# Kernel tuning notes

Hardware: AMD Instinct MI355X
Metric: run time of the kernel (lower is better)

Reference implementation:

```python
import jax, jax.numpy as jnp
import numpy as np

N_NODES = 50000
N_EDGES = 800000
IN_FEATS = 256
HIDDEN = 256
NUM_CLASSES = 64


def setup_inputs() -> dict:
    key = jax.random.key(0)
    k1, k2, k3, k4 = jax.random.split(key, 4)
    features = jax.random.normal(k1, (N_NODES, IN_FEATS), dtype=jnp.float32)
    edge_index = jax.random.randint(k2, (2, N_EDGES), 0, N_NODES, dtype=jnp.int32)
    W1 = jax.random.normal(k3, (IN_FEATS, HIDDEN), dtype=jnp.float32) * (1.0 / np.sqrt(IN_FEATS))
    b1 = jnp.zeros((HIDDEN,), dtype=jnp.float32)
    W2 = jax.random.normal(k4, (HIDDEN, NUM_CLASSES), dtype=jnp.float32) * (1.0 / np.sqrt(HIDDEN))
    b2 = jnp.zeros((NUM_CLASSES,), dtype=jnp.float32)
    return {"features": features, "edge_index": edge_index, "W1": W1, "b1": b1, "W2": W2, "b2": b2}


def reference(features, edge_index, W1, b1, W2, b2):
    # Two-layer GCN: h = A_hat @ relu(A_hat @ X W1 + b1) W2 + b2
    # A_hat uses symmetric degree normalization 1/sqrt(d_src * d_dst)
    N = features.shape[0]
    src, dst = edge_index[0], edge_index[1]
    ones = jnp.ones((src.shape[0],), dtype=features.dtype)
    deg_out = jax.ops.segment_sum(ones, src, num_segments=N)  # out-degree per node
    deg_in = jax.ops.segment_sum(ones, dst, num_segments=N)   # in-degree per node
    inv_sqrt_out = jax.lax.rsqrt(jnp.maximum(deg_out, 1.0))
    inv_sqrt_in = jax.lax.rsqrt(jnp.maximum(deg_in, 1.0))
    edge_norm = (inv_sqrt_out[src] * inv_sqrt_in[dst])[:, None]  # [E,1]

    def gcn_layer(x, W, b):
        h = x @ W                      # transform first (reduces message width)
        msg = h[src] * edge_norm       # [E, out]
        agg = jax.ops.segment_sum(msg, dst, num_segments=N)
        return agg + b

    h = jax.nn.relu(gcn_layer(features, W1, b1))
    return gcn_layer(h, W2, b2)
```

## Files before the change

kernel.cpp:

```cpp
#include <hip/hip_runtime.h>

#define NN 50000
#define MPAD 50048
#define NE 800000
#define SCAN_BLOCKS 49

typedef short short8 __attribute__((ext_vector_type(8)));
typedef float f32x4 __attribute__((ext_vector_type(4)));

__device__ __forceinline__ unsigned short f2bf(float x) {
    unsigned u = __builtin_bit_cast(unsigned, x);
    u += 0x7FFFu + ((u >> 16) & 1u);
    return (unsigned short)(u >> 16);
}
__device__ __forceinline__ float bf2f(unsigned short h) {
    unsigned u = ((unsigned)h) << 16;
    return __builtin_bit_cast(float, u);
}
__device__ __forceinline__ void gld16(const void* g, void* l) {
    __builtin_amdgcn_global_load_lds(
        (const __attribute__((address_space(1))) unsigned int*)g,
        (__attribute__((address_space(3))) unsigned int*)l, 16, 0, 0);
}
__device__ __forceinline__ void nt_store8(void* p, ushort4 v) {
    __builtin_nontemporal_store(__builtin_bit_cast(unsigned long long, v),
                                (unsigned long long*)p);
}


__global__ __launch_bounds__(256) void count_kernel(const int* __restrict__ src,
    const int* __restrict__ dst, int* __restrict__ cnt_out, int* __restrict__ cnt_in, int E)
{
    int e = blockIdx.x * 256 + threadIdx.x;
    if (e < E) {
        atomicAdd(&cnt_out[src[e]], 1);
        atomicAdd(&cnt_in[dst[e]], 1);
    }
}

__global__ __launch_bounds__(256) void scan_kernel(const int* __restrict__ cnt_in,
    const int* __restrict__ cnt_out, int* __restrict__ bsum, int* __restrict__ rs,
    float* __restrict__ inv_out, float* __restrict__ inv_in)
{
    __shared__ int sm[4];
    __shared__ int sprefix;
    const int b = blockIdx.x, tid = threadIdx.x;
    const int lane = tid & 63, wv = tid >> 6;
    int base = b * 1024 + tid * 4;
    int v[4]; int s = 0;
    #pragma unroll
    for (int i = 0; i < 4; ++i) {
        int idx = base + i;
        v[i] = (idx < NN) ? cnt_in[idx] : 0;
        s += v[i];
    }
    int inc = s;
    #pragma unroll
    for (int off = 1; off < 64; off <<= 1) {
        int u = __shfl_up(inc, off, 64);
        if (lane >= off) inc += u;
    }
    if (lane == 63) sm[wv] = inc;
    __syncthreads();
    if (tid == 0) {
        int btot = sm[0] + sm[1] + sm[2] + sm[3];
        atomicExch(&bsum[b], btot + 1);
    }
    if (tid < 64) {
        int pv = 0;
        if (lane < b) {
            int x;
            do { x = atomicAdd(&bsum[lane], 0); } while (x == 0);
            pv = x - 1;
        }
        #pragma unroll
        for (int off = 1; off < 64; off <<= 1) pv += __shfl_xor(pv, off, 64);
        if (lane == 0) sprefix = pv;
    }
    __syncthreads();
    int wo = 0;
    for (int i = 0; i < wv; ++i) wo += sm[i];
    int run = sprefix + wo + (inc - s);
    #pragma unroll
    for (int i = 0; i < 4; ++i) {
        int idx = base + i;
        if (idx < NN) {
            rs[idx] = run; run += v[i];
            inv_in[idx]  = rsqrtf(fmaxf((float)v[i], 1.0f));
            inv_out[idx] = rsqrtf(fmaxf((float)cnt_out[idx], 1.0f));
        }
    }
}

__global__ __launch_bounds__(256) void fill_kernel(const int* __restrict__ src,
    const int* __restrict__ dst, int* __restrict__ rs, int* __restrict__ csr_src, int E)
{
    int e = blockIdx.x * 256 + threadIdx.x;
    if (e < E) {
        int slot = atomicAdd(&rs[dst[e]], 1);
        csr_src[slot] = src[e];
    }
}

__global__ __launch_bounds__(256) void splitW_kernel(const float* __restrict__ W1,
    const float* __restrict__ W2, unsigned short* __restrict__ W1T,
    unsigned short* __restrict__ W2T)
{
    int i = blockIdx.x * 256 + threadIdx.x;
    const float* W; unsigned short* BT; int N; int ii;
    if (i < 256 * 32) { W = W1; BT = W1T; N = 256; ii = i; }
    else if (i < 256 * 32 + 64 * 32) { W = W2; BT = W2T; N = 64; ii = i - 256 * 32; }
    else return;
    int col = ii >> 5, kc = ii & 31;
    short8 hv, lv;
    #pragma unroll
    for (int j = 0; j < 8; ++j) {
        float x = W[(size_t)(kc * 8 + j) * N + col];
        unsigned short h = f2bf(x);
        hv[j] = (short)h;
        lv[j] = (short)f2bf(x - bf2f(h));
    }
    size_t base = (size_t)col * 512;
    size_t o = (kc >> 3) * 64 + (((kc & 7) ^ (col & 7)) * 8);
    *(short8*)&BT[base + o] = hv;
    *(short8*)&BT[base + 256 + o] = lv;
}

__global__ __launch_bounds__(256) void gemm1_fuse_kernel(const float* __restrict__ X,
    const unsigned short* __restrict__ BT, const float* __restrict__ inv_out,
    unsigned short* __restrict__ C, int M)
{
    constexpr int BN = 128, WN = 64, NF = 4;
    __shared__ unsigned short Ash[128 * 64];
    __shared__ unsigned short Asl[128 * 64];
    __shared__ unsigned short Bsh[BN * 64];
    __shared__ unsigned short Bsl[BN * 64];
    const int tid = threadIdx.x;
    const int w = tid >> 6, lane = tid & 63;
    const int wm = w >> 1, wn = w & 1;
    const int r = lane & 15, kg = lane >> 4;
    const int rowbase = blockIdx.x * 128;
    const int colbase = blockIdx.y * BN;

    f32x4 acc[4][NF] = {};

    for (int kb = 0; kb < 4; ++kb) {
        #pragma unroll
        for (int i = 0; i < 4; ++i) {
            int ct = (w * 4 + i) * 64 + lane;
            int row = ct >> 3, c = ct & 7;
            int grow = rowbase + row; if (grow >= NN) grow = NN - 1;
            const float* sp = X + (size_t)grow * 256 + kb * 64 + c * 8;
            float4 x0 = *(const float4*)sp;
            float4 x1 = *(const float4*)(sp + 4);
            float xs[8] = {x0.x, x0.y, x0.z, x0.w, x1.x, x1.y, x1.z, x1.w};
            short8 hv, lv;
            #pragma unroll
            for (int t = 0; t < 8; ++t) {
                unsigned short h = f2bf(xs[t]);
                hv[t] = (short)h;
                lv[t] = (short)f2bf(xs[t] - bf2f(h));
            }
            int dsto = row * 64 + ((c ^ (row & 7)) * 8);
            *(short8*)&Ash[dsto] = hv;
            *(short8*)&Asl[dsto] = lv;
        }
        #pragma unroll
        for (int i = 0; i < 4; ++i) {
            int ct = (w * 4 + i) * 64 + lane;
            int col = ct >> 3, c = ct & 7;
            size_t goff = (size_t)(colbase + col) * 512 + kb * 64 + c * 8;
            gld16(BT + goff, (unsigned short*)Bsh + (size_t)ct * 8);
            gld16(BT + goff + 256, (unsigned short*)Bsl + (size_t)ct * 8);
        }
        __syncthreads();
        #pragma unroll
        for (int ks = 0; ks < 2; ++ks) {
            short8 ahf[4], alf[4];
            #pragma unroll
            for (int mf = 0; mf < 4; ++mf) {
                int row = wm * 64 + mf * 16 + r;
                int lo = row * 64 + (((ks * 4 + kg) ^ (row & 7)) * 8);
                ahf[mf] = *(const short8*)&Ash[lo];
                alf[mf] = *(const short8*)&Asl[lo];
            }
            #pragma unroll
            for (int nf = 0; nf < NF; ++nf) {
                int col = wn * WN + nf * 16 + r;
                int lo = col * 64 + (((ks * 4 + kg) ^ (col & 7)) * 8);
                short8 bh = *(const short8*)&Bsh[lo];
                short8 bl = *(const short8*)&Bsl[lo];
                #pragma unroll
                for (int mf = 0; mf < 4; ++mf) {
                    acc[mf][nf] = __builtin_amdgcn_mfma_f32_16x16x32_bf16(ahf[mf], bh, acc[mf][nf], 0, 0, 0);
                    acc[mf][nf] = __builtin_amdgcn_mfma_f32_16x16x32_bf16(alf[mf], bh, acc[mf][nf], 0, 0, 0);
                    acc[mf][nf] = __builtin_amdgcn_mfma_f32_16x16x32_bf16(ahf[mf], bl, acc[mf][nf], 0, 0, 0);
                }
            }
        }
        __syncthreads();
    }

    #pragma unroll
    for (int mf = 0; mf < 4; ++mf) {
        #pragma unroll
        for (int reg = 0; reg < 4; ++reg) {
            int orow = rowbase + wm * 64 + mf * 16 + kg * 4 + reg;
            if (orow >= M) continue;
            float sc = inv_out[orow];
            #pragma unroll
            for (int nf = 0; nf < NF; ++nf) {
                int ocol = colbase + wn * WN + nf * 16 + r;
                C[(size_t)orow * 256 + ocol] = f2bf(acc[mf][nf][reg] * sc);
            }
        }
    }
}

__global__ __launch_bounds__(256) void gemm2_kernel(
    const unsigned short* __restrict__ Ah, const unsigned short* __restrict__ Al,
    const unsigned short* __restrict__ BT, const float* __restrict__ inv_out,
    unsigned short* __restrict__ C, int M)
{
    constexpr int BN = 64, WN = 32, NF = 2, BI = 2;
    __shared__ unsigned short Ash[128 * 64];
    __shared__ unsigned short Asl[128 * 64];
    __shared__ unsigned short Bsh[BN * 64];
    __shared__ unsigned short Bsl[BN * 64];
    const int tid = threadIdx.x;
    const int w = tid >> 6, lane = tid & 63;
    const int wm = w >> 1, wn = w & 1;
    const int r = lane & 15, kg = lane >> 4;
    const int rowbase = blockIdx.x * 128;

    f32x4 acc[4][NF] = {};

    for (int kb = 0; kb < 4; ++kb) {
        #pragma unroll
        for (int i = 0; i < 4; ++i) {
            int ct = (w * 4 + i) * 64 + lane;
            int row = ct >> 3, c = ct & 7;
            size_t goff = (size_t)(rowbase + row) * 256 + kb * 64 + c * 8;
            gld16(Ah + goff, (unsigned short*)Ash + (size_t)ct * 8);
            gld16(Al + goff, (unsigned short*)Asl + (size_t)ct * 8);
        }
        #pragma unroll
        for (int i = 0; i < BI; ++i) {
            int ct = (w * BI + i) * 64 + lane;
            int col = ct >> 3, c = ct & 7;
            size_t goff = (size_t)col * 512 + kb * 64 + c * 8;
            gld16(BT + goff, (unsigned short*)Bsh + (size_t)ct * 8);
            gld16(BT + goff + 256, (unsigned short*)Bsl + (size_t)ct * 8);
        }
        __syncthreads();
        #pragma unroll
        for (int ks = 0; ks < 2; ++ks) {
            short8 ahf[4], alf[4];
            #pragma unroll
            for (int mf = 0; mf < 4; ++mf) {
                int row = wm * 64 + mf * 16 + r;
                int lo = row * 64 + (((ks * 4 + kg) ^ (row & 7)) * 8);
                ahf[mf] = *(const short8*)&Ash[lo];
                alf[mf] = *(const short8*)&Asl[lo];
            }
            #pragma unroll
            for (int nf = 0; nf < NF; ++nf) {
                int col = wn * WN + nf * 16 + r;
                int lo = col * 64 + (((ks * 4 + kg) ^ (col & 7)) * 8);
                short8 bh = *(const short8*)&Bsh[lo];
                short8 bl = *(const short8*)&Bsl[lo];
                #pragma unroll
                for (int mf = 0; mf < 4; ++mf) {
                    acc[mf][nf] = __builtin_amdgcn_mfma_f32_16x16x32_bf16(ahf[mf], bh, acc[mf][nf], 0, 0, 0);
                    acc[mf][nf] = __builtin_amdgcn_mfma_f32_16x16x32_bf16(alf[mf], bh, acc[mf][nf], 0, 0, 0);
                    acc[mf][nf] = __builtin_amdgcn_mfma_f32_16x16x32_bf16(ahf[mf], bl, acc[mf][nf], 0, 0, 0);
                }
            }
        }
        __syncthreads();
    }

    #pragma unroll
    for (int mf = 0; mf < 4; ++mf) {
        #pragma unroll
        for (int reg = 0; reg < 4; ++reg) {
            int orow = rowbase + wm * 64 + mf * 16 + kg * 4 + reg;
            if (orow >= M) continue;
            float sc = inv_out[orow];
            #pragma unroll
            for (int nf = 0; nf < NF; ++nf) {
                int ocol = wn * WN + nf * 16 + r;
                C[(size_t)orow * 64 + ocol] = f2bf(acc[mf][nf][reg] * sc);
            }
        }
    }
}

__global__ __launch_bounds__(256) void gather256_kernel(const unsigned short* __restrict__ t1,
    const int* __restrict__ csr_src, const int* __restrict__ rs,
    const float* __restrict__ inv_in, const float* __restrict__ b1,
    unsigned short* __restrict__ Ah2, unsigned short* __restrict__ Al2)
{
    int n = (int)((blockIdx.x * 256 + threadIdx.x) >> 6);
    int lane = threadIdx.x & 63;
    if (n >= NN) return;
    int begin = (n == 0) ? 0 : rs[n - 1];
    int end = rs[n];
    float a0 = 0.f, a1 = 0.f, a2 = 0.f, a3 = 0.f;
    int j = begin;
    for (; j + 8 <= end; j += 8) {
        int s0 = csr_src[j],     s1 = csr_src[j + 1], s2 = csr_src[j + 2], s3 = csr_src[j + 3];
        int s4 = csr_src[j + 4], s5 = csr_src[j + 5], s6 = csr_src[j + 6], s7 = csr_src[j + 7];
        ushort4 v0 = *(const ushort4*)&t1[(size_t)s0 * 256 + lane * 4];
        ushort4 v1 = *(const ushort4*)&t1[(size_t)s1 * 256 + lane * 4];
        ushort4 v2 = *(const ushort4*)&t1[(size_t)s2 * 256 + lane * 4];
        ushort4 v3 = *(const ushort4*)&t1[(size_t)s3 * 256 + lane * 4];
        ushort4 v4 = *(const ushort4*)&t1[(size_t)s4 * 256 + lane * 4];
        ushort4 v5 = *(const ushort4*)&t1[(size_t)s5 * 256 + lane * 4];
        ushort4 v6 = *(const ushort4*)&t1[(size_t)s6 * 256 + lane * 4];
        ushort4 v7 = *(const ushort4*)&t1[(size_t)s7 * 256 + lane * 4];
        a0 += bf2f(v0.x); a1 += bf2f(v0.y); a2 += bf2f(v0.z); a3 += bf2f(v0.w);
        a0 += bf2f(v1.x); a1 += bf2f(v1.y); a2 += bf2f(v1.z); a3 += bf2f(v1.w);
        a0 += bf2f(v2.x); a1 += bf2f(v2.y); a2 += bf2f(v2.z); a3 += bf2f(v2.w);
        a0 += bf2f(v3.x); a1 += bf2f(v3.y); a2 += bf2f(v3.z); a3 += bf2f(v3.w);
        a0 += bf2f(v4.x); a1 += bf2f(v4.y); a2 += bf2f(v4.z); a3 += bf2f(v4.w);
        a0 += bf2f(v5.x); a1 += bf2f(v5.y); a2 += bf2f(v5.z); a3 += bf2f(v5.w);
        a0 += bf2f(v6.x); a1 += bf2f(v6.y); a2 += bf2f(v6.z); a3 += bf2f(v6.w);
        a0 += bf2f(v7.x); a1 += bf2f(v7.y); a2 += bf2f(v7.z); a3 += bf2f(v7.w);
    }
    for (; j < end; ++j) {
        int s = csr_src[j];
        ushort4 v = *(const ushort4*)&t1[(size_t)s * 256 + lane * 4];
        a0 += bf2f(v.x); a1 += bf2f(v.y); a2 += bf2f(v.z); a3 += bf2f(v.w);
    }
    float win = inv_in[n];
    int f0 = lane * 4;
    float4 bb = *(const float4*)&b1[f0];
    float x0 = fmaxf(fmaf(a0, win, bb.x), 0.f);
    float x1 = fmaxf(fmaf(a1, win, bb.y), 0.f);
    float x2 = fmaxf(fmaf(a2, win, bb.z), 0.f);
    float x3 = fmaxf(fmaf(a3, win, bb.w), 0.f);
    unsigned short h0 = f2bf(x0), h1 = f2bf(x1), h2 = f2bf(x2), h3 = f2bf(x3);
    ushort4 hv = {h0, h1, h2, h3};
    ushort4 lv = {f2bf(x0 - bf2f(h0)), f2bf(x1 - bf2f(h1)),
                  f2bf(x2 - bf2f(h2)), f2bf(x3 - bf2f(h3))};
    int kb = f0 >> 6, c = (f0 >> 3) & 7, e = f0 & 7;
    size_t off = (size_t)n * 256 + kb * 64 + ((c ^ (n & 7)) * 8) + e;
    nt_store8(&Ah2[off], hv);
    nt_store8(&Al2[off], lv);
}

__global__ __launch_bounds__(256) void gather64_kernel(const unsigned short* __restrict__ t2,
    const int* __restrict__ csr_src, const int* __restrict__ rs,
    const float* __restrict__ inv_in, const float* __restrict__ b2,
    float* __restrict__ out)
{
    int n = (int)((blockIdx.x * 256 + threadIdx.x) >> 6);
    int lane = threadIdx.x & 63;
    if (n >= NN) return;
    int begin = (n == 0) ? 0 : rs[n - 1];
    int end = rs[n];
    float acc = 0.f;
    int j = begin;
    for (; j + 8 <= end; j += 8) {
        int s0 = csr_src[j],     s1 = csr_src[j + 1], s2 = csr_src[j + 2], s3 = csr_src[j + 3];
        int s4 = csr_src[j + 4], s5 = csr_src[j + 5], s6 = csr_src[j + 6], s7 = csr_src[j + 7];
        float v0 = bf2f(t2[(size_t)s0 * 64 + lane]);
        float v1 = bf2f(t2[(size_t)s1 * 64 + lane]);
        float v2 = bf2f(t2[(size_t)s2 * 64 + lane]);
        float v3 = bf2f(t2[(size_t)s3 * 64 + lane]);
        float v4 = bf2f(t2[(size_t)s4 * 64 + lane]);
        float v5 = bf2f(t2[(size_t)s5 * 64 + lane]);
        float v6 = bf2f(t2[(size_t)s6 * 64 + lane]);
        float v7 = bf2f(t2[(size_t)s7 * 64 + lane]);
        acc += v0; acc += v1; acc += v2; acc += v3;
        acc += v4; acc += v5; acc += v6; acc += v7;
    }
    for (; j < end; ++j) {
        int s = csr_src[j];
        acc += bf2f(t2[(size_t)s * 64 + lane]);
    }
    float o = fmaf(acc, inv_in[n], b2[lane]);
    __builtin_nontemporal_store(o, &out[(size_t)n * 64 + lane]);
}

extern "C" void kernel_launch(void* const* d_in, const int* in_sizes, int n_in,
                              void* d_out, int out_size, void* d_ws, size_t ws_size,
                              hipStream_t stream)
{
    const float* features = (const float*)d_in[0];
    const int*   edge_index = (const int*)d_in[1];
    const float* W1 = (const float*)d_in[2];
    const float* b1 = (const float*)d_in[3];
    const float* W2 = (const float*)d_in[4];
    const float* b2 = (const float*)d_in[5];
    float* out = (float*)d_out;
    const int* src = edge_index;
    const int* dst = edge_index + NE;

    char* p = (char*)d_ws;
    int* cnt_out = (int*)p;            p += (size_t)NN * 4;
    int* cnt_in  = (int*)p;            p += (size_t)NN * 4;
    int* bsum    = (int*)p;            p += 64 * 4;
    float* inv_out = (float*)p;        p += (size_t)NN * 4;
    float* inv_in  = (float*)p;        p += (size_t)NN * 4;
    int* rs      = (int*)p;            p += (size_t)NN * 4;
    int* csr_src = (int*)p;            p += (size_t)NE * 4;
    unsigned short* W1T = (unsigned short*)p;  p += (size_t)256 * 512 * 2;
    unsigned short* W2T = (unsigned short*)p;  p += (size_t)64 * 512 * 2;
    unsigned short* t1  = (unsigned short*)p;  p += (size_t)NN * 256 * 2;
    unsigned short* Ah2 = (unsigned short*)p;  p += (size_t)MPAD * 256 * 2;
    unsigned short* Al2 = (unsigned short*)p;  p += (size_t)MPAD * 256 * 2;
    unsigned short* t2  = (unsigned short*)p;  p += (size_t)NN * 64 * 2;

    hipMemsetAsync(cnt_out, 0, (2 * (size_t)NN + 64) * sizeof(int), stream);

    count_kernel<<<(NE + 255) / 256, 256, 0, stream>>>(src, dst, cnt_out, cnt_in, NE);
    scan_kernel<<<SCAN_BLOCKS, 256, 0, stream>>>(cnt_in, cnt_out, bsum, rs, inv_out, inv_in);
    fill_kernel<<<(NE + 255) / 256, 256, 0, stream>>>(src, dst, rs, csr_src, NE);

    splitW_kernel<<<(320 * 32 + 255) / 256, 256, 0, stream>>>(W1, W2, W1T, W2T);

    gemm1_fuse_kernel<<<dim3(MPAD / 128, 2), 256, 0, stream>>>(
        features, W1T, inv_out, t1, NN);

    gather256_kernel<<<(NN * 64 + 255) / 256, 256, 0, stream>>>(
        t1, csr_src, rs, inv_in, b1, Ah2, Al2);

    gemm2_kernel<<<MPAD / 128, 256, 0, stream>>>(
        Ah2, Al2, W2T, inv_out, t2, NN);

    gather64_kernel<<<(NN * 64 + 255) / 256, 256, 0, stream>>>(
        t2, csr_src, rs, inv_in, b2, out);
}
```

Before: 301.4 us.

## Fold weight split into count kernel, split gather256 into chunks, nontemporal index loads

Moves the weight hi/lo bf16 split into the edge-count kernel so one launch goes away. The layer-1 gather is now issued as three launches over node ranges instead of one, presumably to change cache behaviour or scheduling. CSR index loads in both gathers use nontemporal loads so the index stream does not displace the gathered feature rows from cache. The chunked launches add launch overhead and drain gaps between the chunks.

```diff
diff --git a/kernel.cpp b/kernel.cpp
--- a/kernel.cpp
+++ b/kernel.cpp
@@ -26,15 +26,38 @@
     __builtin_nontemporal_store(__builtin_bit_cast(unsigned long long, v),
                                 (unsigned long long*)p);
 }
-
+__device__ __forceinline__ int nt_load_i(const int* p) {
+    return __builtin_nontemporal_load(p);
+}
 
 __global__ __launch_bounds__(256) void count_kernel(const int* __restrict__ src,
-    const int* __restrict__ dst, int* __restrict__ cnt_out, int* __restrict__ cnt_in, int E)
+    const int* __restrict__ dst, int* __restrict__ cnt_out, int* __restrict__ cnt_in,
+    const float* __restrict__ W1, const float* __restrict__ W2,
+    unsigned short* __restrict__ W1T, unsigned short* __restrict__ W2T, int E)
 {
     int e = blockIdx.x * 256 + threadIdx.x;
     if (e < E) {
         atomicAdd(&cnt_out[src[e]], 1);
         atomicAdd(&cnt_in[dst[e]], 1);
+    }
+    int i = blockIdx.x * 256 + threadIdx.x;
+    if (i < 320 * 32) {
+        const float* W; unsigned short* BT; int N; int ii;
+        if (i < 256 * 32) { W = W1; BT = W1T; N = 256; ii = i; }
+        else { W = W2; BT = W2T; N = 64; ii = i - 256 * 32; }
+        int col = ii >> 5, kc = ii & 31;
+        short8 hv, lv;
+        #pragma unroll
+        for (int j = 0; j < 8; ++j) {
+            float x = W[(size_t)(kc * 8 + j) * N + col];
+            unsigned short h = f2bf(x);
+            hv[j] = (short)h;
+            lv[j] = (short)f2bf(x - bf2f(h));
+        }
+        size_t base = (size_t)col * 512;
+        size_t o = (kc >> 3) * 64 + (((kc & 7) ^ (col & 7)) * 8);
+        *(short8*)&BT[base + o] = hv;
+        *(short8*)&BT[base + 256 + o] = lv;
     }
 }
 
@@ -102,30 +125,6 @@
     }
 }
 
-__global__ __launch_bounds__(256) void splitW_kernel(const float* __restrict__ W1,
-    const float* __restrict__ W2, unsigned short* __restrict__ W1T,
-    unsigned short* __restrict__ W2T)
-{
-    int i = blockIdx.x * 256 + threadIdx.x;
-    const float* W; unsigned short* BT; int N; int ii;
-    if (i < 256 * 32) { W = W1; BT = W1T; N = 256; ii = i; }
-    else if (i < 256 * 32 + 64 * 32) { W = W2; BT = W2T; N = 64; ii = i - 256 * 32; }
-    else return;
-    int col = ii >> 5, kc = ii & 31;
-    short8 hv, lv;
-    #pragma unroll
-    for (int j = 0; j < 8; ++j) {
-        float x = W[(size_t)(kc * 8 + j) * N + col];
-        unsigned short h = f2bf(x);
-        hv[j] = (short)h;
-        lv[j] = (short)f2bf(x - bf2f(h));
-    }
-    size_t base = (size_t)col * 512;
-    size_t o = (kc >> 3) * 64 + (((kc & 7) ^ (col & 7)) * 8);
-    *(short8*)&BT[base + o] = hv;
-    *(short8*)&BT[base + 256 + o] = lv;
-}
-
 __global__ __launch_bounds__(256) void gemm1_fuse_kernel(const float* __restrict__ X,
     const unsigned short* __restrict__ BT, const float* __restrict__ inv_out,
     unsigned short* __restrict__ C, int M)
@@ -299,18 +298,20 @@
 __global__ __launch_bounds__(256) void gather256_kernel(const unsigned short* __restrict__ t1,
     const int* __restrict__ csr_src, const int* __restrict__ rs,
     const float* __restrict__ inv_in, const float* __restrict__ b1,
-    unsigned short* __restrict__ Ah2, unsigned short* __restrict__ Al2)
-{
-    int n = (int)((blockIdx.x * 256 + threadIdx.x) >> 6);
+    unsigned short* __restrict__ Ah2, unsigned short* __restrict__ Al2, int n0, int n1)
+{
+    int n = n0 + (int)((blockIdx.x * 256 + threadIdx.x) >> 6);
     int lane = threadIdx.x & 63;
-    if (n >= NN) return;
+    if (n >= n1) return;
     int begin = (n == 0) ? 0 : rs[n - 1];
     int end = rs[n];
     float a0 = 0.f, a1 = 0.f, a2 = 0.f, a3 = 0.f;
     int j = begin;
     for (; j + 8 <= end; j += 8) {
-        int s0 = csr_src[j],     s1 = csr_src[j + 1], s2 = csr_src[j + 2], s3 = csr_src[j + 3];
-        int s4 = csr_src[j + 4], s5 = csr_src[j + 5], s6 = csr_src[j + 6], s7 = csr_src[j + 7];
+        int s0 = nt_load_i(csr_src + j),     s1 = nt_load_i(csr_src + j + 1);
+        int s2 = nt_load_i(csr_src + j + 2), s3 = nt_load_i(csr_src + j + 3);
+        int s4 = nt_load_i(csr_src + j + 4), s5 = nt_load_i(csr_src + j + 5);
+        int s6 = nt_load_i(csr_src + j + 6), s7 = nt_load_i(csr_src + j + 7);
         ushort4 v0 = *(const ushort4*)&t1[(size_t)s0 * 256 + lane * 4];
         ushort4 v1 = *(const ushort4*)&t1[(size_t)s1 * 256 + lane * 4];
         ushort4 v2 = *(const ushort4*)&t1[(size_t)s2 * 256 + lane * 4];
@@ -363,8 +364,10 @@
     float acc = 0.f;
     int j = begin;
     for (; j + 8 <= end; j += 8) {
-        int s0 = csr_src[j],     s1 = csr_src[j + 1], s2 = csr_src[j + 2], s3 = csr_src[j + 3];
-        int s4 = csr_src[j + 4], s5 = csr_src[j + 5], s6 = csr_src[j + 6], s7 = csr_src[j + 7];
+        int s0 = nt_load_i(csr_src + j),     s1 = nt_load_i(csr_src + j + 1);
+        int s2 = nt_load_i(csr_src + j + 2), s3 = nt_load_i(csr_src + j + 3);
+        int s4 = nt_load_i(csr_src + j + 4), s5 = nt_load_i(csr_src + j + 5);
+        int s6 = nt_load_i(csr_src + j + 6), s7 = nt_load_i(csr_src + j + 7);
         float v0 = bf2f(t2[(size_t)s0 * 64 + lane]);
         float v1 = bf2f(t2[(size_t)s1 * 64 + lane]);
         float v2 = bf2f(t2[(size_t)s2 * 64 + lane]);
@@ -415,17 +418,21 @@
 
     hipMemsetAsync(cnt_out, 0, (2 * (size_t)NN + 64) * sizeof(int), stream);
 
-    count_kernel<<<(NE + 255) / 256, 256, 0, stream>>>(src, dst, cnt_out, cnt_in, NE);
+    count_kernel<<<(NE + 255) / 256, 256, 0, stream>>>(
+        src, dst, cnt_out, cnt_in, W1, W2, W1T, W2T, NE);
     scan_kernel<<<SCAN_BLOCKS, 256, 0, stream>>>(cnt_in, cnt_out, bsum, rs, inv_out, inv_in);
     fill_kernel<<<(NE + 255) / 256, 256, 0, stream>>>(src, dst, rs, csr_src, NE);
 
-    splitW_kernel<<<(320 * 32 + 255) / 256, 256, 0, stream>>>(W1, W2, W1T, W2T);
-
     gemm1_fuse_kernel<<<dim3(MPAD / 128, 2), 256, 0, stream>>>(
         features, W1T, inv_out, t1, NN);
 
-    gather256_kernel<<<(NN * 64 + 255) / 256, 256, 0, stream>>>(
-        t1, csr_src, rs, inv_in, b1, Ah2, Al2);
+    const int NS = 16672;
+    for (int s0 = 0; s0 < NN; s0 += NS) {
+        int s1 = s0 + NS < NN ? s0 + NS : NN;
+        int nodes = s1 - s0;
+        gather256_kernel<<<(nodes * 64 + 255) / 256, 256, 0, stream>>>(
+            t1, csr_src, rs, inv_in, b1, Ah2, Al2, s0, s1);
+    }
 
     gemm2_kernel<<<MPAD / 128, 256, 0, stream>>>(
         Ah2, Al2, W2T, inv_out, t2, NN);
```

After: 312.8 us. 3.8% more time.
